# Kernel tuning notes

Measured on AMD Instinct MI355X. Metric: run time of the kernel, lower is better.

The kernel has to match this reference:

```python
import jax, jax.numpy as jnp
import numpy as np

B, N, D = 8, 256, 3          # batch, particles, spatial dims
H = 64                        # hidden_nf (channels)
L = 4                         # num_layers
ENC = 3                       # atom_type, aa_type, aa_pos
IN_NF = ENC + 1               # + time
COORDS_RANGE = 15.0 / L       # tanh=True -> coords_range/n_layers
E = B * N * N                 # fully-connected edges per batch graph


def _linear(key, fin, fout):
    k1, k2 = jax.random.split(key)
    s = 1.0 / np.sqrt(fin)
    w = jax.random.uniform(k1, (fout, fin), minval=-s, maxval=s, dtype=jnp.float32)
    b = jax.random.uniform(k2, (fout,), minval=-s, maxval=s, dtype=jnp.float32)
    return w, b


def setup_inputs() -> dict:
    key = jax.random.key(0)
    ks = jax.random.split(key, 64)
    inp = {
        "t": jax.random.uniform(ks[0], (B, 1), dtype=jnp.float32),
        "x": jax.random.normal(ks[1], (B, N * D), dtype=jnp.float32),
        "atom_type": jax.random.uniform(ks[2], (B, N), dtype=jnp.float32),
        "aa_type": jax.random.uniform(ks[3], (B, N), dtype=jnp.float32),
        "aa_pos": jax.random.uniform(ks[4], (B, N), dtype=jnp.float32),
        "node_mask": jnp.ones((B, N), dtype=jnp.float32),
    }
    inp["emb_w"], inp["emb_b"] = _linear(ks[5], IN_NF, H)
    specs = [("edge_w1", "edge_b1", 2 * H + 2, H), ("edge_w2", "edge_b2", H, H),
             ("node_w1", "node_b1", 2 * H, H), ("node_w2", "node_b2", H, H),
             ("coord_w1", "coord_b1", H, H), ("att_w", "att_b", H, 1)]
    kk = 6
    for wn, bn, fin, fout in specs:
        ws, bs = [], []
        for _ in range(L):
            w, b = _linear(ks[kk], fin, fout); kk += 1
            ws.append(w); bs.append(b)
        inp[wn] = jnp.stack(ws); inp[bn] = jnp.stack(bs)
    # final coord layer: Linear(H,1,bias=False), xavier gain 0.001
    inp["coord_w2"] = jax.random.normal(ks[kk], (L, 1, H), dtype=jnp.float32) * 0.001
    return inp


def _edges():
    idx = jnp.arange(N)
    row_in = jnp.repeat(idx, N)
    col_in = jnp.tile(idx, N)
    off = (jnp.arange(B) * N)[:, None]
    row = (off + row_in[None, :]).reshape(-1)
    col = (off + col_in[None, :]).reshape(-1)
    return row, col


def reference(t, x, atom_type, aa_type, aa_pos, node_mask,
              emb_w, emb_b, edge_w1, edge_b1, edge_w2, edge_b2,
              node_w1, node_b1, node_w2, node_b2,
              coord_w1, coord_b1, att_w, att_b, coord_w2):
    silu = jax.nn.silu
    row, col = _edges()
    nm = node_mask.reshape(B * N, 1)
    # edge mask: pairwise node mask with diagonal (self-loop) removed
    em = ((node_mask[:, :, None] * node_mask[:, None, :])
          * (1.0 - jnp.eye(N, dtype=jnp.float32))).reshape(E, 1)

    x0 = x.reshape(B * N, D) * nm
    tt = jnp.broadcast_to(t, (B, N)).reshape(B * N, 1) * nm
    h = jnp.stack([atom_type, aa_type, aa_pos], axis=-1).reshape(B * N, ENC) * nm
    h = jnp.concatenate([h, tt], axis=1)                      # [BN, 4]
    edge_attr0 = jnp.sum((x0[row] - x0[col]) ** 2, axis=1, keepdims=True)  # [E,1]

    h = h @ emb_w.T + emb_b                                   # embedding -> [BN, H]
    coord = x0
    for l in range(L):
        diff = coord[row] - coord[col]                        # [E, D]
        radial = jnp.sum(diff ** 2, axis=1, keepdims=True)    # [E, 1]
        diff = diff / (jnp.sqrt(radial + 1e-8) + 1.0)         # norm_diff
        m = jnp.concatenate([h[row], h[col], radial, edge_attr0], axis=1)
        m = silu(m @ edge_w1[l].T + edge_b1[l])
        m = silu(m @ edge_w2[l].T + edge_b2[l])               # [E, H]
        m = m * jax.nn.sigmoid(m @ att_w[l].T + att_b[l]) * em
        phi = jnp.tanh(silu(m @ coord_w1[l].T + coord_b1[l]) @ coord_w2[l].T)
        trans = diff * phi * COORDS_RANGE * em                # [E, D]
        coord = (coord + jax.ops.segment_sum(trans, row, num_segments=B * N)) * nm
        agg = jax.ops.segment_sum(m, row, num_segments=B * N)  # [BN, H]
        upd = jnp.concatenate([h, agg], axis=1)
        upd = silu(upd @ node_w1[l].T + node_b1[l]) @ node_w2[l].T + node_b2[l]
        h = (h + upd) * nm                                    # recurrent residual

    vel = (coord - x0) * nm
    vel = vel.reshape(B, N, D)
    nmr = node_mask.reshape(B, N, 1)
    Ns = jnp.sum(nmr, axis=1, keepdims=True)
    vel = vel - (jnp.sum(vel, axis=1, keepdims=True) / Ns) * nmr  # remove_mean_with_mask
    return vel.reshape(B, N * D)
```

## Files before the change

kernel.cpp:

```cpp
#include <hip/hip_runtime.h>

#define CRANGE 3.75f

typedef _Float16 half_t;
typedef __attribute__((ext_vector_type(8))) _Float16 half8;
typedef __attribute__((ext_vector_type(4))) _Float16 half4;
typedef __attribute__((ext_vector_type(4))) float f32x4;

__device__ __forceinline__ float frcp(float x) { return __builtin_amdgcn_rcpf(x); }
__device__ __forceinline__ float fexpn(float x) { return __expf(fminf(x, 20.f)); }
__device__ __forceinline__ float fsilu(float x) { return x * frcp(1.f + fexpn(-x)); }

__device__ __forceinline__ void inv4(float d0, float d1, float d2, float d3, float* o) {
    float p01 = d0 * d1, p23 = d2 * d3;
    float r = frcp(p01 * p23);
    float t01 = p23 * r, t23 = p01 * r;
    o[0] = d1 * t01; o[1] = d0 * t01; o[2] = d3 * t23; o[3] = d2 * t23;
}
__device__ __forceinline__ void silu4(const float* x, float* o) {
    float d0 = 1.f + fexpn(-x[0]), d1 = 1.f + fexpn(-x[1]);
    float d2 = 1.f + fexpn(-x[2]), d3 = 1.f + fexpn(-x[3]);
    float iv[4]; inv4(d0, d1, d2, d3, iv);
    o[0] = x[0] * iv[0]; o[1] = x[1] * iv[1]; o[2] = x[2] * iv[2]; o[3] = x[3] * iv[3];
}

__global__ void k_prep(const float* __restrict__ ew2, const float* __restrict__ cw1,
                       const float* __restrict__ nw1, const float* __restrict__ nw2,
                       const float* __restrict__ ew1,
                       half_t* __restrict__ wf, float* __restrict__ trT) {
    int idx = blockIdx.x * 256 + threadIdx.x;
    if (idx < 4096) {
        int lane = idx & 63;
        int g = (idx >> 6) & 7;
        int mat = (idx >> 9) & 1;
        int l = idx >> 10;
        int mt = g >> 1, kc = g & 1;
        int c = lane & 15, qq = lane >> 4;
        const float* W = (mat ? cw1 : ew2) + l * 4096;
        int row = 16 * mt + c;
        int k0 = 32 * kc + 8 * qq;
        half8 pk;
#pragma unroll
        for (int j = 0; j < 8; ++j) pk[j] = (half_t)W[row * 64 + k0 + j];
        ((half8*)wf)[idx] = pk;
    }
    int tid2 = idx - 4096;
    if (tid2 >= 0 && tid2 < 81920) {
        int l = tid2 / 20480, r = tid2 % 20480;
        float v;
        if (r < 8192)       { int k = r >> 6,        c = r & 63; v = nw1[l * 8192 + c * 128 + k]; }
        else if (r < 12288) { int r2 = r - 8192,  k = r2 >> 6, c = r2 & 63; v = nw2[l * 4096 + c * 64 + k]; }
        else if (r < 16384) { int r2 = r - 12288, k = r2 >> 6, c = r2 & 63; v = ew1[l * 8320 + c * 130 + k]; }
        else                { int r2 = r - 16384, k = r2 >> 6, c = r2 & 63; v = ew1[l * 8320 + c * 130 + 64 + k]; }
        trT[l * 20480 + r] = v;
    }
}

__global__ void k_init(const float* __restrict__ t, const float* __restrict__ x,
                       const float* __restrict__ at, const float* __restrict__ aa,
                       const float* __restrict__ ap, const float* __restrict__ nm,
                       const float* __restrict__ embw, const float* __restrict__ embb,
                       const float* __restrict__ ew1aT0, const float* __restrict__ ew1bT0,
                       const float* __restrict__ eb1_0,
                       float* __restrict__ h, float* __restrict__ Hr, float* __restrict__ HcA,
                       float* __restrict__ x0, float* __restrict__ cA) {
    int n = blockIdx.x, c = threadIdx.x;
    __shared__ float sh[64];
    float m = nm[n]; int b = n >> 8;
    float i0 = at[n] * m, i1 = aa[n] * m, i2 = ap[n] * m, i3 = t[b] * m;
    float4 w = ((const float4*)embw)[c];
    float hv = w.x * i0 + w.y * i1 + w.z * i2 + w.w * i3 + embb[c];
    sh[c] = hv; h[n * 64 + c] = hv;
    if (c < 3) { float v = x[n * 3 + c] * m; x0[n * 3 + c] = v; cA[n * 3 + c] = v; }
    __syncthreads();
    float a = eb1_0[c], bb = 0.f;
#pragma unroll
    for (int k = 0; k < 64; ++k) {
        float hk = sh[k];
        a  += ew1aT0[k * 64 + c] * hk;
        bb += ew1bT0[k * 64 + c] * hk;
    }
    Hr[n * 64 + c] = a;
    HcA[n * 64 + c] = bb;
}

__global__ __launch_bounds__(256, 4) void k_edge(
    const float* __restrict__ coordIn, const float* __restrict__ x0,
    float* __restrict__ Hr, const float* __restrict__ Hc,
    const float* __restrict__ ew1, const float* __restrict__ eb2,
    const float* __restrict__ cb1, const float* __restrict__ attw,
    const float* __restrict__ attb, const float* __restrict__ cw2,
    const float* __restrict__ nm, const half_t* __restrict__ wf2,
    const half_t* __restrict__ wf1,
    float* __restrict__ hbuf,
    const float* __restrict__ nw1T, const float* __restrict__ nw2T,
    const float* __restrict__ nb1, const float* __restrict__ nb2,
    const float* __restrict__ ew1aTn, const float* __restrict__ ew1bTn,
    const float* __restrict__ eb1n,
    float* __restrict__ HcO, float* __restrict__ coordOut)
{
    __shared__ __align__(16) half_t sV[4][4096];
    __shared__ __align__(16) float sGeo[4][64][4];
    __shared__ float sHr[64], sWr[64], sWe[64], sB2[64], sBc1[64], sAttw[64], sWc2[64];
    __shared__ float sAgg[64];
    __shared__ float sCoord[3];

    const int i = blockIdx.x, b = i >> 8, ir = i & 255;
    const int t = threadIdx.x, wv = t >> 6, e = t & 63;
    const int q = e >> 4, c = e & 15;
    const int col = (b << 8) + t;

    if (t < 64) {
        sHr[t] = Hr[i * 64 + t];
        sWr[t] = ew1[t * 130 + 128];
        sWe[t] = ew1[t * 130 + 129];
        sB2[t] = eb2[t]; sBc1[t] = cb1[t]; sAttw[t] = attw[t]; sWc2[t] = cw2[t];
        sAgg[t] = 0.f;
    }
    if (t == 64) { sCoord[0] = 0.f; sCoord[1] = 0.f; sCoord[2] = 0.f; }
    float attb0 = attb[0];
    float nmi = nm[i];

    float dx = coordIn[i*3+0] - coordIn[col*3+0];
    float dy = coordIn[i*3+1] - coordIn[col*3+1];
    float dz = coordIn[i*3+2] - coordIn[col*3+2];
    float radial = dx*dx + dy*dy + dz*dz;
    float inv = frcp(__builtin_amdgcn_sqrtf(radial + 1e-8f) + 1.f);
    float ex = x0[i*3+0] - x0[col*3+0];
    float ey = x0[i*3+1] - x0[col*3+1];
    float ez = x0[i*3+2] - x0[col*3+2];
    float e0 = ex*ex + ey*ey + ez*ez;
    float em = nmi * nm[col] * ((t == ir) ? 0.f : 1.f);

    __syncthreads();

    {
        float4 g4 = make_float4(dx*inv, dy*inv, dz*inv, em);
        *(float4*)&sGeo[wv][e][0] = g4;
    }

    half_t* mybuf = (half_t*)sV[wv];
    const float4* hcv = (const float4*)(Hc + col * 64);
#pragma unroll
    for (int s = 0; s < 8; ++s) {
        float4 ha = hcv[2*s], hb = hcv[2*s+1];
        float z[8], so[8];
        z[0]=ha.x; z[1]=ha.y; z[2]=ha.z; z[3]=ha.w;
        z[4]=hb.x; z[5]=hb.y; z[6]=hb.z; z[7]=hb.w;
#pragma unroll
        for (int u = 0; u < 8; ++u) {
            int k = 8*s + u;
            z[u] = sHr[k] + z[u] + radial * sWr[k] + e0 * sWe[k];
        }
        silu4(z, so); silu4(z + 4, so + 4);
        half8 pk;
#pragma unroll
        for (int u = 0; u < 8; ++u) pk[u] = (half_t)so[u];
        int f = q * 2 + (s >> 2);
        *(half8*)&mybuf[f * 512 + ((s & 3) * 16 + c) * 8] = pk;
    }

    const half8* bv = (const half8*)mybuf;
    f32x4 acc[4][4];
#pragma unroll
    for (int mt = 0; mt < 4; ++mt) {
        int row0 = 16*mt + 4*q;
#pragma unroll
        for (int nt = 0; nt < 4; ++nt)
#pragma unroll
            for (int r = 0; r < 4; ++r) acc[mt][nt][r] = sB2[row0 + r];
    }
    {
        const half8* a2v = (const half8*)wf2;
        half8 a2[8];
#pragma unroll
        for (int g = 0; g < 8; ++g) a2[g] = a2v[g * 64 + e];
#pragma unroll
        for (int nt = 0; nt < 4; ++nt) {
            half8 b0 = bv[(nt*2+0)*64 + e];
            half8 b1 = bv[(nt*2+1)*64 + e];
#pragma unroll
            for (int mt = 0; mt < 4; ++mt) {
                acc[mt][nt] = __builtin_amdgcn_mfma_f32_16x16x32_f16(a2[mt*2+0], b0, acc[mt][nt], 0, 0, 0);
                acc[mt][nt] = __builtin_amdgcn_mfma_f32_16x16x32_f16(a2[mt*2+1], b1, acc[mt][nt], 0, 0, 0);
            }
        }
    }

    float attp[4] = {0.f, 0.f, 0.f, 0.f};
#pragma unroll
    for (int mt = 0; mt < 4; ++mt) {
        int row0 = 16*mt + 4*q;
#pragma unroll
        for (int nt = 0; nt < 4; ++nt) {
            float z[4], so[4];
#pragma unroll
            for (int r = 0; r < 4; ++r) z[r] = acc[mt][nt][r];
            silu4(z, so);
#pragma unroll
            for (int r = 0; r < 4; ++r) {
                acc[mt][nt][r] = so[r];
                attp[nt] += so[r] * sAttw[row0 + r];
            }
        }
    }
#pragma unroll
    for (int nt = 0; nt < 4; ++nt) {
        float v = attp[nt];
        v += __shfl_xor(v, 16);
        v += __shfl_xor(v, 32);
        attp[nt] = v;
    }
    float scale[4];
    {
        float d0 = 1.f + fexpn(-(attp[0] + attb0));
        float d1 = 1.f + fexpn(-(attp[1] + attb0));
        float d2 = 1.f + fexpn(-(attp[2] + attb0));
        float d3 = 1.f + fexpn(-(attp[3] + attb0));
        float iv[4]; inv4(d0, d1, d2, d3, iv);
#pragma unroll
        for (int nt = 0; nt < 4; ++nt) scale[nt] = iv[nt] * sGeo[wv][16*nt + c][3];
    }

    float aggp[4][4];
#pragma unroll
    for (int mt = 0; mt < 4; ++mt)
#pragma unroll
        for (int r = 0; r < 4; ++r) aggp[mt][r] = 0.f;
#pragma unroll
    for (int mt = 0; mt < 4; ++mt) {
        int kbase = 16*mt + 4*q;
        int fof = ((kbase >> 5) * 512) + (((kbase >> 3) & 3) * 128) + (kbase & 7);
#pragma unroll
        for (int nt = 0; nt < 4; ++nt) {
            half4 pk;
#pragma unroll
            for (int r = 0; r < 4; ++r) {
                float v = acc[mt][nt][r] * scale[nt];
                aggp[mt][r] += v;
                pk[r] = (half_t)v;
            }
            *(half4*)&mybuf[nt*1024 + fof + c*8] = pk;
        }
    }

    half8 a1[8];
    {
        const half8* a1v = (const half8*)wf1;
#pragma unroll
        for (int g = 0; g < 8; ++g) a1[g] = a1v[g * 64 + e];
    }

#pragma unroll
    for (int mt = 0; mt < 4; ++mt)
#pragma unroll
        for (int r = 0; r < 4; ++r) {
            float v = aggp[mt][r];
            v += __shfl_xor(v, 1); v += __shfl_xor(v, 2);
            v += __shfl_xor(v, 4); v += __shfl_xor(v, 8);
            if (c == 0) atomicAdd(&sAgg[16*mt + 4*q + r], v);
        }

    f32x4 acc2[4][4];
#pragma unroll
    for (int mt = 0; mt < 4; ++mt) {
        int row0 = 16*mt + 4*q;
#pragma unroll
        for (int nt = 0; nt < 4; ++nt)
#pragma unroll
            for (int r = 0; r < 4; ++r) acc2[mt][nt][r] = sBc1[row0 + r];
    }
#pragma unroll
    for (int nt = 0; nt < 4; ++nt) {
        half8 b0 = bv[(nt*2+0)*64 + e];
        half8 b1 = bv[(nt*2+1)*64 + e];
#pragma unroll
        for (int mt = 0; mt < 4; ++mt) {
            acc2[mt][nt] = __builtin_amdgcn_mfma_f32_16x16x32_f16(a1[mt*2+0], b0, acc2[mt][nt], 0, 0, 0);
            acc2[mt][nt] = __builtin_amdgcn_mfma_f32_16x16x32_f16(a1[mt*2+1], b1, acc2[mt][nt], 0, 0, 0);
        }
    }

    float php[4] = {0.f, 0.f, 0.f, 0.f};
#pragma unroll
    for (int mt = 0; mt < 4; ++mt) {
        int row0 = 16*mt + 4*q;
#pragma unroll
        for (int nt = 0; nt < 4; ++nt) {
            float z[4], so[4];
#pragma unroll
            for (int r = 0; r < 4; ++r) z[r] = acc2[mt][nt][r];
            silu4(z, so);
#pragma unroll
            for (int r = 0; r < 4; ++r) php[nt] += so[r] * sWc2[row0 + r];
        }
    }
#pragma unroll
    for (int nt = 0; nt < 4; ++nt) {
        float v = php[nt];
        v += __shfl_xor(v, 16);
        v += __shfl_xor(v, 32);
        php[nt] = v;
    }
    float tnh[4];
    {
        float d0 = fexpn(2.f * php[0]) + 1.f;
        float d1 = fexpn(2.f * php[1]) + 1.f;
        float d2 = fexpn(2.f * php[2]) + 1.f;
        float d3 = fexpn(2.f * php[3]) + 1.f;
        float iv[4]; inv4(d0, d1, d2, d3, iv);
#pragma unroll
        for (int nt = 0; nt < 4; ++nt) tnh[nt] = 1.f - 2.f * iv[nt];
    }
    float tx = 0.f, ty = 0.f, tz = 0.f;
#pragma unroll
    for (int nt = 0; nt < 4; ++nt) {
        float4 g4 = *(float4*)&sGeo[wv][16*nt + c][0];
        float tr = tnh[nt] * CRANGE * g4.w;
        tx += g4.x * tr; ty += g4.y * tr; tz += g4.z * tr;
    }
    tx += __shfl_xor(tx, 1); tx += __shfl_xor(tx, 2); tx += __shfl_xor(tx, 4); tx += __shfl_xor(tx, 8);
    ty += __shfl_xor(ty, 1); ty += __shfl_xor(ty, 2); ty += __shfl_xor(ty, 4); ty += __shfl_xor(ty, 8);
    tz += __shfl_xor(tz, 1); tz += __shfl_xor(tz, 2); tz += __shfl_xor(tz, 4); tz += __shfl_xor(tz, 8);
    if (e == 0) {
        atomicAdd(&sCoord[0], tx);
        atomicAdd(&sCoord[1], ty);
        atomicAdd(&sCoord[2], tz);
    }

    __syncthreads();

    float* sT   = (float*)&sV[0][0];
    float* sIn  = sT;
    float* sP   = sT + 128;
    float* sU   = sT + 384;
    float* sHn  = sT + 448;
    float* sPB  = sT + 512;

    if (t < 64) sIn[t] = hbuf[i * 64 + t];
    else if (t < 128) sIn[t] = sAgg[t - 64];
    if (t >= 128 && t < 131) {
        int d = t - 128;
        coordOut[i * 3 + d] = (coordIn[i * 3 + d] + sCoord[d]) * nmi;
    }
    __syncthreads();

    const int cc = t & 63, p = t >> 6;
    {
        float a = 0.f;
        const float* w = nw1T + (p * 32) * 64 + cc;
#pragma unroll
        for (int k = 0; k < 32; ++k) a += w[k * 64] * sIn[p * 32 + k];
        sP[p * 64 + cc] = a;
    }
    __syncthreads();
    if (t < 64) sU[t] = fsilu(sP[t] + sP[64 + t] + sP[128 + t] + sP[192 + t] + nb1[t]);
    __syncthreads();
    {
        float a = 0.f;
        const float* w = nw2T + (p * 16) * 64 + cc;
#pragma unroll
        for (int k = 0; k < 16; ++k) a += w[k * 64] * sU[p * 16 + k];
        sP[p * 64 + cc] = a;
    }
    __syncthreads();
    if (t < 64) {
        float hn = (sIn[t] + sP[t] + sP[64 + t] + sP[128 + t] + sP[192 + t] + nb2[t]) * nmi;
        hbuf[i * 64 + t] = hn;
        sHn[t] = hn;
    }
    __syncthreads();
    {
        float a = 0.f, b2 = 0.f;
        const float* wa = ew1aTn + (p * 16) * 64 + cc;
        const float* wb = ew1bTn + (p * 16) * 64 + cc;
#pragma unroll
        for (int k = 0; k < 16; ++k) {
            float hv = sHn[p * 16 + k];
            a  += wa[k * 64] * hv;
            b2 += wb[k * 64] * hv;
        }
        sP[p * 64 + cc] = a;
        sPB[p * 64 + cc] = b2;
    }
    __syncthreads();
    if (t < 64) {
        Hr[i * 64 + t]  = sP[t] + sP[64 + t] + sP[128 + t] + sP[192 + t] + eb1n[t];
        HcO[i * 64 + t] = sPB[t] + sPB[64 + t] + sPB[128 + t] + sPB[192 + t];
    }
}

__global__ void k_final(const float* __restrict__ coord, const float* __restrict__ x0,
                        const float* __restrict__ nm, float* __restrict__ out) {
    int b = blockIdx.x;
    int t = threadIdx.x;
    int i = b * 256 + t;
    int lane = t & 63;
    float m = nm[i];
    float vx = (coord[i * 3 + 0] - x0[i * 3 + 0]) * m;
    float vy = (coord[i * 3 + 1] - x0[i * 3 + 1]) * m;
    float vz = (coord[i * 3 + 2] - x0[i * 3 + 2]) * m;
    __shared__ float red[4];
    if (t < 4) red[t] = 0.f;
    __syncthreads();
    float sx = vx, sy = vy, sz = vz, sn = m;
#pragma unroll
    for (int off = 1; off < 64; off <<= 1) {
        sx += __shfl_xor(sx, off);
        sy += __shfl_xor(sy, off);
        sz += __shfl_xor(sz, off);
        sn += __shfl_xor(sn, off);
    }
    if (lane == 0) {
        atomicAdd(&red[0], sx); atomicAdd(&red[1], sy);
        atomicAdd(&red[2], sz); atomicAdd(&red[3], sn);
    }
    __syncthreads();
    float invNs = frcp(red[3]);
    out[b * 768 + t * 3 + 0] = vx - red[0] * invNs * m;
    out[b * 768 + t * 3 + 1] = vy - red[1] * invNs * m;
    out[b * 768 + t * 3 + 2] = vz - red[2] * invNs * m;
}

extern "C" void kernel_launch(void* const* d_in, const int* in_sizes, int n_in,
                              void* d_out, int out_size, void* d_ws, size_t ws_size,
                              hipStream_t stream) {
    const float* t_in    = (const float*)d_in[0];
    const float* x_in    = (const float*)d_in[1];
    const float* at_in   = (const float*)d_in[2];
    const float* aa_in   = (const float*)d_in[3];
    const float* ap_in   = (const float*)d_in[4];
    const float* nm_in   = (const float*)d_in[5];
    const float* emb_w   = (const float*)d_in[6];
    const float* emb_b   = (const float*)d_in[7];
    const float* edge_w1 = (const float*)d_in[8];
    const float* edge_b1 = (const float*)d_in[9];
    const float* edge_w2 = (const float*)d_in[10];
    const float* edge_b2 = (const float*)d_in[11];
    const float* node_w1 = (const float*)d_in[12];
    const float* node_b1 = (const float*)d_in[13];
    const float* node_w2 = (const float*)d_in[14];
    const float* node_b2 = (const float*)d_in[15];
    const float* coord_w1= (const float*)d_in[16];
    const float* coord_b1= (const float*)d_in[17];
    const float* att_w   = (const float*)d_in[18];
    const float* att_b   = (const float*)d_in[19];
    const float* coord_w2= (const float*)d_in[20];

    float* ws  = (float*)d_ws;
    float* h   = ws;
    float* Hr  = h + 131072;
    float* HcA = Hr + 131072;
    float* HcB = HcA + 131072;
    float* x0  = HcB + 131072;
    float* cA  = x0 + 6144;
    float* cB  = cA + 6144;
    float* base = cB + 6144;
    half_t* wf = (half_t*)base;
    float* trT = base + 16384;

    float* out = (float*)d_out;

    k_prep<<<336, 256, 0, stream>>>(edge_w2, coord_w1, node_w1, node_w2, edge_w1, wf, trT);
    k_init<<<2048, 64, 0, stream>>>(t_in, x_in, at_in, aa_in, ap_in, nm_in, emb_w, emb_b,
                                    trT + 12288, trT + 16384, edge_b1,
                                    h, Hr, HcA, x0, cA);

    for (int l = 0; l < 4; ++l) {
        const float* ew1 = edge_w1 + l * 8320;
        const float* eb2 = edge_b2 + l * 64;
        const float* cb1 = coord_b1 + l * 64;
        const float* aw  = att_w + l * 64;
        const float* ab  = att_b + l;
        const float* cw2 = coord_w2 + l * 64;
        const float* nb1 = node_b1 + l * 64;
        const float* nb2 = node_b2 + l * 64;

        const float* trL = trT + l * 20480;
        int ln = (l + 1) & 3;
        const float* trN = trT + ln * 20480;

        const float* cin  = (l & 1) ? cB : cA;
        float*       cout = (l & 1) ? cA : cB;
        const float* HcR  = (l & 1) ? HcB : HcA;
        float*       HcW  = (l & 1) ? HcA : HcB;

        k_edge<<<2048, 256, 0, stream>>>(cin, x0, Hr, HcR, ew1, eb2, cb1,
                                         aw, ab, cw2, nm_in,
                                         wf + l * 8192, wf + l * 8192 + 4096,
                                         h, trL, trL + 8192, nb1, nb2,
                                         trN + 12288, trN + 16384, edge_b1 + ln * 64,
                                         HcW, cout);
    }

    k_final<<<8, 256, 0, stream>>>(cA, x0, nm_in, out);
}
```

Measured before the change: 304.1 us.

## Split edge kernel across 512 threads with two lanes per edge

The per-row edge kernel now launches 512 threads instead of 256. Each 64-lane wave handles 32 edges, and the two halves of the wave split the 64 input channels of the first edge-layer SiLU. The MFMA tiles per wave drop from 4 to 2 column tiles, and the node-update matvecs are split 8 ways instead of 4. The goal is more waves per row and less work and register use per wave, which should improve latency hiding. The cost is duplicated geometry loads, wf2 weight loads spread across more waves, and wider reductions.

```diff
diff --git a/kernel.cpp b/kernel.cpp
--- a/kernel.cpp
+++ b/kernel.cpp
@@ -16,6 +16,10 @@
     float r = frcp(p01 * p23);
     float t01 = p23 * r, t23 = p01 * r;
     o[0] = d1 * t01; o[1] = d0 * t01; o[2] = d3 * t23; o[3] = d2 * t23;
+}
+__device__ __forceinline__ void inv2(float d0, float d1, float* o) {
+    float r = frcp(d0 * d1);
+    o[0] = d1 * r; o[1] = d0 * r;
 }
 __device__ __forceinline__ void silu4(const float* x, float* o) {
     float d0 = 1.f + fexpn(-x[0]), d1 = 1.f + fexpn(-x[1]);
@@ -84,7 +88,7 @@
     HcA[n * 64 + c] = bb;
 }
 
-__global__ __launch_bounds__(256, 4) void k_edge(
+__global__ __launch_bounds__(512, 4) void k_edge(
     const float* __restrict__ coordIn, const float* __restrict__ x0,
     float* __restrict__ Hr, const float* __restrict__ Hc,
     const float* __restrict__ ew1, const float* __restrict__ eb2,
@@ -99,16 +103,19 @@
     const float* __restrict__ eb1n,
     float* __restrict__ HcO, float* __restrict__ coordOut)
 {
-    __shared__ __align__(16) half_t sV[4][4096];
-    __shared__ __align__(16) float sGeo[4][64][4];
+    __shared__ __align__(16) half_t sV[8][2048];
+    __shared__ __align__(16) float sGeo[8][32][4];
     __shared__ float sHr[64], sWr[64], sWe[64], sB2[64], sBc1[64], sAttw[64], sWc2[64];
     __shared__ float sAgg[64];
     __shared__ float sCoord[3];
 
     const int i = blockIdx.x, b = i >> 8, ir = i & 255;
-    const int t = threadIdx.x, wv = t >> 6, e = t & 63;
-    const int q = e >> 4, c = e & 15;
-    const int col = (b << 8) + t;
+    const int t = threadIdx.x;
+    const int wv = t >> 6, L = t & 63;
+    const int q = L >> 4, c = L & 15;
+    const int se = L & 31, hh = L >> 5;
+    const int src = (wv << 5) + se;
+    const int col = (b << 8) + src;
 
     if (t < 64) {
         sHr[t] = Hr[i * 64 + t];
@@ -130,69 +137,71 @@
     float ey = x0[i*3+1] - x0[col*3+1];
     float ez = x0[i*3+2] - x0[col*3+2];
     float e0 = ex*ex + ey*ey + ez*ez;
-    float em = nmi * nm[col] * ((t == ir) ? 0.f : 1.f);
-
-    __syncthreads();
-
-    {
+    float em = nmi * nm[col] * ((src == ir) ? 0.f : 1.f);
+
+    __syncthreads();
+
+    if (hh == 0) {
         float4 g4 = make_float4(dx*inv, dy*inv, dz*inv, em);
-        *(float4*)&sGeo[wv][e][0] = g4;
+        *(float4*)&sGeo[wv][se][0] = g4;
     }
 
     half_t* mybuf = (half_t*)sV[wv];
-    const float4* hcv = (const float4*)(Hc + col * 64);
-#pragma unroll
-    for (int s = 0; s < 8; ++s) {
-        float4 ha = hcv[2*s], hb = hcv[2*s+1];
+    const half8* bv = (const half8*)mybuf;
+    const float4* hcv = (const float4*)(Hc + col * 64 + hh * 32);
+
+    half8 a2[8];
+    {
+        const half8* a2v = (const half8*)wf2;
+#pragma unroll
+        for (int g = 0; g < 8; ++g) a2[g] = a2v[g * 64 + L];
+    }
+
+    const int ntw = se >> 4, cse = se & 15;
+#pragma unroll
+    for (int s2 = 0; s2 < 4; ++s2) {
+        float4 ha = hcv[2*s2], hb = hcv[2*s2+1];
         float z[8], so[8];
         z[0]=ha.x; z[1]=ha.y; z[2]=ha.z; z[3]=ha.w;
         z[4]=hb.x; z[5]=hb.y; z[6]=hb.z; z[7]=hb.w;
 #pragma unroll
         for (int u = 0; u < 8; ++u) {
-            int k = 8*s + u;
+            int k = hh*32 + 8*s2 + u;
             z[u] = sHr[k] + z[u] + radial * sWr[k] + e0 * sWe[k];
         }
         silu4(z, so); silu4(z + 4, so + 4);
         half8 pk;
 #pragma unroll
         for (int u = 0; u < 8; ++u) pk[u] = (half_t)so[u];
-        int f = q * 2 + (s >> 2);
-        *(half8*)&mybuf[f * 512 + ((s & 3) * 16 + c) * 8] = pk;
-    }
-
-    const half8* bv = (const half8*)mybuf;
-    f32x4 acc[4][4];
+        *(half8*)&mybuf[(ntw*2 + hh) * 512 + (s2 * 16 + cse) * 8] = pk;
+    }
+
+    f32x4 acc[4][2];
 #pragma unroll
     for (int mt = 0; mt < 4; ++mt) {
         int row0 = 16*mt + 4*q;
 #pragma unroll
-        for (int nt = 0; nt < 4; ++nt)
+        for (int nt = 0; nt < 2; ++nt)
 #pragma unroll
             for (int r = 0; r < 4; ++r) acc[mt][nt][r] = sB2[row0 + r];
     }
-    {
-        const half8* a2v = (const half8*)wf2;
-        half8 a2[8];
-#pragma unroll
-        for (int g = 0; g < 8; ++g) a2[g] = a2v[g * 64 + e];
-#pragma unroll
-        for (int nt = 0; nt < 4; ++nt) {
-            half8 b0 = bv[(nt*2+0)*64 + e];
-            half8 b1 = bv[(nt*2+1)*64 + e];
-#pragma unroll
-            for (int mt = 0; mt < 4; ++mt) {
-                acc[mt][nt] = __builtin_amdgcn_mfma_f32_16x16x32_f16(a2[mt*2+0], b0, acc[mt][nt], 0, 0, 0);
-                acc[mt][nt] = __builtin_amdgcn_mfma_f32_16x16x32_f16(a2[mt*2+1], b1, acc[mt][nt], 0, 0, 0);
-            }
-        }
-    }
-
-    float attp[4] = {0.f, 0.f, 0.f, 0.f};
+#pragma unroll
+    for (int nt = 0; nt < 2; ++nt) {
+        half8 b0 = bv[(nt*2+0)*64 + L];
+        half8 b1 = bv[(nt*2+1)*64 + L];
+#pragma unroll
+        for (int mt = 0; mt < 4; ++mt) {
+            acc[mt][nt] = __builtin_amdgcn_mfma_f32_16x16x32_f16(a2[mt*2+0], b0, acc[mt][nt], 0, 0, 0);
+            acc[mt][nt] = __builtin_amdgcn_mfma_f32_16x16x32_f16(a2[mt*2+1], b1, acc[mt][nt], 0, 0, 0);
+        }
+    }
+
+    float attp[2] = {0.f, 0.f};
 #pragma unroll
     for (int mt = 0; mt < 4; ++mt) {
         int row0 = 16*mt + 4*q;
 #pragma unroll
-        for (int nt = 0; nt < 4; ++nt) {
+        for (int nt = 0; nt < 2; ++nt) {
             float z[4], so[4];
 #pragma unroll
             for (int r = 0; r < 4; ++r) z[r] = acc[mt][nt][r];
@@ -205,21 +214,19 @@
         }
     }
 #pragma unroll
-    for (int nt = 0; nt < 4; ++nt) {
+    for (int nt = 0; nt < 2; ++nt) {
         float v = attp[nt];
         v += __shfl_xor(v, 16);
         v += __shfl_xor(v, 32);
         attp[nt] = v;
     }
-    float scale[4];
+    float scale[2];
     {
         float d0 = 1.f + fexpn(-(attp[0] + attb0));
         float d1 = 1.f + fexpn(-(attp[1] + attb0));
-        float d2 = 1.f + fexpn(-(attp[2] + attb0));
-        float d3 = 1.f + fexpn(-(attp[3] + attb0));
-        float iv[4]; inv4(d0, d1, d2, d3, iv);
-#pragma unroll
-        for (int nt = 0; nt < 4; ++nt) scale[nt] = iv[nt] * sGeo[wv][16*nt + c][3];
+        float iv[2]; inv2(d0, d1, iv);
+        scale[0] = iv[0] * sGeo[wv][c][3];
+        scale[1] = iv[1] * sGeo[wv][16 + c][3];
     }
 
     float aggp[4][4];
@@ -232,7 +239,7 @@
         int kbase = 16*mt + 4*q;
         int fof = ((kbase >> 5) * 512) + (((kbase >> 3) & 3) * 128) + (kbase & 7);
 #pragma unroll
-        for (int nt = 0; nt < 4; ++nt) {
+        for (int nt = 0; nt < 2; ++nt) {
             half4 pk;
 #pragma unroll
             for (int r = 0; r < 4; ++r) {
@@ -248,7 +255,7 @@
     {
         const half8* a1v = (const half8*)wf1;
 #pragma unroll
-        for (int g = 0; g < 8; ++g) a1[g] = a1v[g * 64 + e];
+        for (int g = 0; g < 8; ++g) a1[g] = a1v[g * 64 + L];
     }
 
 #pragma unroll
@@ -261,19 +268,19 @@
             if (c == 0) atomicAdd(&sAgg[16*mt + 4*q + r], v);
         }
 
-    f32x4 acc2[4][4];
+    f32x4 acc2[4][2];
 #pragma unroll
     for (int mt = 0; mt < 4; ++mt) {
         int row0 = 16*mt + 4*q;
 #pragma unroll
-        for (int nt = 0; nt < 4; ++nt)
+        for (int nt = 0; nt < 2; ++nt)
 #pragma unroll
             for (int r = 0; r < 4; ++r) acc2[mt][nt][r] = sBc1[row0 + r];
     }
 #pragma unroll
-    for (int nt = 0; nt < 4; ++nt) {
-        half8 b0 = bv[(nt*2+0)*64 + e];
-        half8 b1 = bv[(nt*2+1)*64 + e];
+    for (int nt = 0; nt < 2; ++nt) {
+        half8 b0 = bv[(nt*2+0)*64 + L];
+        half8 b1 = bv[(nt*2+1)*64 + L];
 #pragma unroll
         for (int mt = 0; mt < 4; ++mt) {
             acc2[mt][nt] = __builtin_amdgcn_mfma_f32_16x16x32_f16(a1[mt*2+0], b0, acc2[mt][nt], 0, 0, 0);
@@ -281,12 +288,12 @@
         }
     }
 
-    float php[4] = {0.f, 0.f, 0.f, 0.f};
+    float php[2] = {0.f, 0.f};
 #pragma unroll
     for (int mt = 0; mt < 4; ++mt) {
         int row0 = 16*mt + 4*q;
 #pragma unroll
-        for (int nt = 0; nt < 4; ++nt) {
+        for (int nt = 0; nt < 2; ++nt) {
             float z[4], so[4];
 #pragma unroll
             for (int r = 0; r < 4; ++r) z[r] = acc2[mt][nt][r];
@@ -296,25 +303,23 @@
         }
     }
 #pragma unroll
-    for (int nt = 0; nt < 4; ++nt) {
+    for (int nt = 0; nt < 2; ++nt) {
         float v = php[nt];
         v += __shfl_xor(v, 16);
         v += __shfl_xor(v, 32);
         php[nt] = v;
     }
-    float tnh[4];
+    float tnh[2];
     {
         float d0 = fexpn(2.f * php[0]) + 1.f;
         float d1 = fexpn(2.f * php[1]) + 1.f;
-        float d2 = fexpn(2.f * php[2]) + 1.f;
-        float d3 = fexpn(2.f * php[3]) + 1.f;
-        float iv[4]; inv4(d0, d1, d2, d3, iv);
-#pragma unroll
-        for (int nt = 0; nt < 4; ++nt) tnh[nt] = 1.f - 2.f * iv[nt];
+        float iv[2]; inv2(d0, d1, iv);
+        tnh[0] = 1.f - 2.f * iv[0];
+        tnh[1] = 1.f - 2.f * iv[1];
     }
     float tx = 0.f, ty = 0.f, tz = 0.f;
 #pragma unroll
-    for (int nt = 0; nt < 4; ++nt) {
+    for (int nt = 0; nt < 2; ++nt) {
         float4 g4 = *(float4*)&sGeo[wv][16*nt + c][0];
         float tr = tnh[nt] * CRANGE * g4.w;
         tx += g4.x * tr; ty += g4.y * tr; tz += g4.z * tr;
@@ -322,7 +327,7 @@
     tx += __shfl_xor(tx, 1); tx += __shfl_xor(tx, 2); tx += __shfl_xor(tx, 4); tx += __shfl_xor(tx, 8);
     ty += __shfl_xor(ty, 1); ty += __shfl_xor(ty, 2); ty += __shfl_xor(ty, 4); ty += __shfl_xor(ty, 8);
     tz += __shfl_xor(tz, 1); tz += __shfl_xor(tz, 2); tz += __shfl_xor(tz, 4); tz += __shfl_xor(tz, 8);
-    if (e == 0) {
+    if (L == 0) {
         atomicAdd(&sCoord[0], tx);
         atomicAdd(&sCoord[1], ty);
         atomicAdd(&sCoord[2], tz);
@@ -333,9 +338,9 @@
     float* sT   = (float*)&sV[0][0];
     float* sIn  = sT;
     float* sP   = sT + 128;
-    float* sU   = sT + 384;
-    float* sHn  = sT + 448;
-    float* sPB  = sT + 512;
+    float* sU   = sT + 640;
+    float* sHn  = sT + 704;
+    float* sPB  = sT + 768;
 
     if (t < 64) sIn[t] = hbuf[i * 64 + t];
     else if (t < 128) sIn[t] = sAgg[t - 64];
@@ -348,35 +353,43 @@
     const int cc = t & 63, p = t >> 6;
     {
         float a = 0.f;
-        const float* w = nw1T + (p * 32) * 64 + cc;
-#pragma unroll
-        for (int k = 0; k < 32; ++k) a += w[k * 64] * sIn[p * 32 + k];
+        const float* w = nw1T + (p * 16) * 64 + cc;
+#pragma unroll
+        for (int k = 0; k < 16; ++k) a += w[k * 64] * sIn[p * 16 + k];
         sP[p * 64 + cc] = a;
     }
     __syncthreads();
-    if (t < 64) sU[t] = fsilu(sP[t] + sP[64 + t] + sP[128 + t] + sP[192 + t] + nb1[t]);
+    if (t < 64) {
+        float s = nb1[t];
+#pragma unroll
+        for (int j = 0; j < 8; ++j) s += sP[j * 64 + t];
+        sU[t] = fsilu(s);
+    }
     __syncthreads();
     {
         float a = 0.f;
-        const float* w = nw2T + (p * 16) * 64 + cc;
-#pragma unroll
-        for (int k = 0; k < 16; ++k) a += w[k * 64] * sU[p * 16 + k];
+        const float* w = nw2T + (p * 8) * 64 + cc;
+#pragma unroll
+        for (int k = 0; k < 8; ++k) a += w[k * 64] * sU[p * 8 + k];
         sP[p * 64 + cc] = a;
     }
     __syncthreads();
     if (t < 64) {
-        float hn = (sIn[t] + sP[t] + sP[64 + t] + sP[128 + t] + sP[192 + t] + nb2[t]) * nmi;
+        float s = sIn[t] + nb2[t];
+#pragma unroll
+        for (int j = 0; j < 8; ++j) s += sP[j * 64 + t];
+        float hn = s * nmi;
         hbuf[i * 64 + t] = hn;
         sHn[t] = hn;
     }
     __syncthreads();
     {
         float a = 0.f, b2 = 0.f;
-        const float* wa = ew1aTn + (p * 16) * 64 + cc;
-        const float* wb = ew1bTn + (p * 16) * 64 + cc;
-#pragma unroll
-        for (int k = 0; k < 16; ++k) {
-            float hv = sHn[p * 16 + k];
+        const float* wa = ew1aTn + (p * 8) * 64 + cc;
+        const float* wb = ew1bTn + (p * 8) * 64 + cc;
+#pragma unroll
+        for (int k = 0; k < 8; ++k) {
+            float hv = sHn[p * 8 + k];
             a  += wa[k * 64] * hv;
             b2 += wb[k * 64] * hv;
         }
@@ -385,8 +398,11 @@
     }
     __syncthreads();
     if (t < 64) {
-        Hr[i * 64 + t]  = sP[t] + sP[64 + t] + sP[128 + t] + sP[192 + t] + eb1n[t];
-        HcO[i * 64 + t] = sPB[t] + sPB[64 + t] + sPB[128 + t] + sPB[192 + t];
+        float sa = eb1n[t], sb = 0.f;
+#pragma unroll
+        for (int j = 0; j < 8; ++j) { sa += sP[j * 64 + t]; sb += sPB[j * 64 + t]; }
+        Hr[i * 64 + t]  = sa;
+        HcO[i * 64 + t] = sb;
     }
 }
 
@@ -485,7 +501,7 @@
         const float* HcR  = (l & 1) ? HcB : HcA;
         float*       HcW  = (l & 1) ? HcA : HcB;
 
-        k_edge<<<2048, 256, 0, stream>>>(cin, x0, Hr, HcR, ew1, eb2, cb1,
+        k_edge<<<2048, 512, 0, stream>>>(cin, x0, Hr, HcR, ew1, eb2, cb1,
                                          aw, ab, cw2, nm_in,
                                          wf + l * 8192, wf + l * 8192 + 4096,
                                          h, trL, trL + 8192, nb1, nb2,
```

Measured after the change: 335.8 us. 1.1x slower.
